# Kernel tuning notes

Measured on AMD Instinct MI355X. Metric: run time of the kernel, lower is better.

The kernel has to match this reference:

```python
import jax, jax.numpy as jnp
import numpy as np

L = 4        # routed layers
E = 12       # experts
NH = 4       # attention heads
C = 256      # hidden_dim
M = 128      # mlp_dim
TOPK = 1
LN_EPS = 1e-5


def setup_inputs() -> dict:
    key = jax.random.key(0)
    ks = jax.random.split(key, 16)
    B, H, W = 128, 14, 14

    def w(k, shape, s=0.02):
        return jax.random.normal(k, shape, dtype=jnp.float32) * s

    return {
        'stem_out': jax.random.normal(ks[0], (B, C, H, W), dtype=jnp.float32),
        'gate_w': w(ks[1], (L, C, E)), 'gate_b': jnp.zeros((L, E), jnp.float32),
        'ln1_g': jnp.ones((L, E, C), jnp.float32), 'ln1_b': jnp.zeros((L, E, C), jnp.float32),
        'wq': w(ks[2], (L, E, C, C)), 'bq': jnp.zeros((L, E, C), jnp.float32),
        'wk': w(ks[3], (L, E, C, C)), 'bk': jnp.zeros((L, E, C), jnp.float32),
        'wv': w(ks[4], (L, E, C, C)), 'bv': jnp.zeros((L, E, C), jnp.float32),
        'wo': w(ks[5], (L, E, C, C)), 'bo': jnp.zeros((L, E, C), jnp.float32),
        'ln2_g': jnp.ones((L, E, C), jnp.float32), 'ln2_b': jnp.zeros((L, E, C), jnp.float32),
        'w1': w(ks[6], (L, E, C, M)), 'b1': jnp.zeros((L, E, M), jnp.float32),
        'w2': w(ks[7], (L, E, M, C)), 'b2': jnp.zeros((L, E, C), jnp.float32),
    }


def _ln(x, g, b):
    mu = x.mean(axis=-1, keepdims=True)
    var = ((x - mu) ** 2).mean(axis=-1, keepdims=True)
    return (x - mu) * jax.lax.rsqrt(var + LN_EPS) * g + b


def _vit_block(x, p):
    # x: (B, H, W, C); p: per-expert params (no expert axis)
    B, H, W, Cc = x.shape
    d = Cc // NH
    h = _ln(x, p['g1'], p['bb1'])
    q = h @ p['wq'] + p['bq']
    k = h @ p['wk'] + p['bk']
    v = h @ p['wv'] + p['bv']

    def split(t):  # (B,H,W,C) -> (B, NH, H, W, d)
        return jnp.transpose(t.reshape(B, H, W, NH, d), (0, 3, 1, 2, 4))

    q, k, v = split(q), split(k), split(v)
    # attention is computed PER ROW h (over the W axis), matching the
    # original matmul(q, k.transpose(-2,-1)) on b n h w d tensors
    scale = jnp.asarray(d, x.dtype) ** 0.5
    scores = jnp.einsum('bnhqd,bnhkd->bnhqk', q, k) / scale
    attn = jax.nn.softmax(scores, axis=-1)
    o = jnp.einsum('bnhqk,bnhkd->bnhqd', attn, v)
    o = jnp.transpose(o, (0, 2, 3, 1, 4)).reshape(B, H, W, Cc)
    o = o @ p['wo'] + p['bo']
    x = x + o
    m = _ln(x, p['g2'], p['bb2'])
    m = jax.nn.gelu(m @ p['w1'] + p['b1'], approximate=False) @ p['w2'] + p['b2']
    return x + m


def reference(stem_out, gate_w, gate_b, ln1_g, ln1_b, wq, bq, wk, bk, wv, bv,
              wo, bo, ln2_g, ln2_b, w1, b1, w2, b2):
    x = jnp.transpose(stem_out, (0, 2, 3, 1))  # (B, H, W, C)
    B = x.shape[0]
    outputs_map, probs_list, idx_list = [], [], []
    for li in range(L):
        router_in = x.mean(axis=(1, 2))                 # (B, C)
        logits = router_in @ gate_w[li] + gate_b[li]    # (B, E)
        all_probs = jax.nn.softmax(logits, axis=-1)
        tk_p, tk_i = jax.lax.top_k(all_probs, TOPK)
        tk_p = tk_p / (tk_p.sum(axis=-1, keepdims=True) + 1e-8)
        # dense combine weights (B, E): scatter top-k weights per batch row
        w_be = jnp.zeros((B, E), x.dtype).at[jnp.arange(B)[:, None], tk_i].add(tk_p)
        p_li = {'g1': ln1_g[li], 'bb1': ln1_b[li],
                'wq': wq[li], 'bq': bq[li], 'wk': wk[li], 'bk': bk[li],
                'wv': wv[li], 'bv': bv[li], 'wo': wo[li], 'bo': bo[li],
                'g2': ln2_g[li], 'bb2': ln2_b[li],
                'w1': w1[li], 'b1': b1[li], 'w2': w2[li], 'b2': b2[li]}
        expert_outs = jax.vmap(lambda pp: _vit_block(x, pp))(p_li)  # (E,B,H,W,C)
        x = jnp.einsum('ebhwc,be->bhwc', expert_outs, w_be)
        outputs_map.append(jax.lax.stop_gradient(x))
        probs_list.append(all_probs)
        idx_list.append(tk_i)
    return (jnp.stack(outputs_map, axis=0),          # (4, B, H, W, C)
            jnp.concatenate(probs_list, axis=0),     # (4B, E)
            jnp.concatenate(idx_list, axis=0))       # (4B, top_k)
```

## Files before the change

kernel.cpp:

```cpp
#include <hip/hip_runtime.h>
#include <hip/hip_bf16.h>

#define LNUM 4
#define ENUM 12
#define CH 256
#define MLP 128
#define HW 196
#define BNUM 128
#define ROWLEN 14
#define MTOT (BNUM * HW)
#define TM 64
#define MAXTILE 416

#define PK_WQ 0
#define PK_WK 786432
#define PK_WV 1572864
#define PK_WO 2359296
#define PK_W1 3145728
#define PK_W2 3538944
#define PK_TOTAL 3932160

using bf16x8 = __attribute__((ext_vector_type(8))) short;
using f32x4 = __attribute__((ext_vector_type(4))) float;

__device__ inline unsigned short f2bf(float v) {
  __hip_bfloat16 b = __float2bfloat16(v);
  return *reinterpret_cast<unsigned short*>(&b);
}
__device__ inline float bf2f(unsigned short u) {
  union { unsigned int i; float f; } cv;
  cv.i = ((unsigned int)u) << 16;
  return cv.f;
}
__device__ inline void split_bf(float v, unsigned short& hi, unsigned short& lo) {
  hi = f2bf(v);
  lo = f2bf(v - bf2f(hi));
}
__device__ inline void gload16(const void* g, void* l) {
  __builtin_amdgcn_global_load_lds(
      (const __attribute__((address_space(1))) unsigned int*)g,
      (__attribute__((address_space(3))) unsigned int*)l, 16, 0, 0);
}

__global__ __launch_bounds__(256) void transpose_stem(const float* __restrict__ stem,
                                                      float* __restrict__ x) {
  __shared__ float tile[32][33];
  int b = blockIdx.z;
  int c0 = blockIdx.x * 32;
  int p0 = blockIdx.y * 32;
  int tx = threadIdx.x;
  int ty = threadIdx.y;
  for (int i = ty; i < 32; i += 8) {
    int c = c0 + i, p = p0 + tx;
    if (p < HW) tile[i][tx] = stem[(size_t)b * CH * HW + (size_t)c * HW + p];
  }
  __syncthreads();
  for (int i = ty; i < 32; i += 8) {
    int p = p0 + i, c = c0 + tx;
    if (p < HW) x[(size_t)b * HW * CH + (size_t)p * CH + c] = tile[tx][i];
  }
}

__global__ __launch_bounds__(256) void router_kernel(
    const float* __restrict__ x, const float* __restrict__ gate_w,
    const float* __restrict__ gate_b, float* __restrict__ probs_out,
    float* __restrict__ idx_out, float* __restrict__ weight,
    int* __restrict__ eidx, int li) {
  int b = blockIdx.x;
  int c = threadIdx.x;
  const float* xb = x + (size_t)b * HW * CH;
  float s = 0.f;
  for (int p = 0; p < HW; ++p) s += xb[(size_t)p * CH + c];
  __shared__ float r[CH];
  r[c] = s * (1.0f / (float)HW);
  __syncthreads();
  __shared__ float logits[ENUM];
  if (c < ENUM) {
    float acc = gate_b[li * ENUM + c];
    for (int k = 0; k < CH; ++k)
      acc += r[k] * gate_w[((size_t)li * CH + k) * ENUM + c];
    logits[c] = acc;
  }
  __syncthreads();
  if (c == 0) {
    float mx = logits[0]; int am = 0;
    for (int e = 1; e < ENUM; ++e) if (logits[e] > mx) { mx = logits[e]; am = e; }
    float pr[ENUM]; float den = 0.f;
    for (int e = 0; e < ENUM; ++e) { pr[e] = expf(logits[e] - mx); den += pr[e]; }
    float inv = 1.0f / den;
    for (int e = 0; e < ENUM; ++e) pr[e] *= inv;
    for (int e = 0; e < ENUM; ++e)
      probs_out[(size_t)(li * BNUM + b) * ENUM + e] = pr[e];
    idx_out[li * BNUM + b] = (float)am;
    float pmax = pr[am];
    weight[b] = pmax / (pmax + 1e-8f);
    eidx[b] = am;
  }
}

__global__ void route_plan(const int* __restrict__ eidx, int* __restrict__ perm,
                           int* __restrict__ tile_e, int* __restrict__ tile_row0,
                           int* __restrict__ tile_rows) {
  __shared__ int cnt[ENUM], start[ENUM];
  int t = threadIdx.x;
  if (t < ENUM) {
    int c = 0;
    for (int b = 0; b < BNUM; ++b) if (eidx[b] == t) ++c;
    cnt[t] = c;
  }
  __syncthreads();
  if (t == 0) {
    int s = 0;
    for (int e = 0; e < ENUM; ++e) { start[e] = s; s += cnt[e]; }
  }
  __syncthreads();
  if (t < ENUM) {
    int pos = start[t];
    for (int b = 0; b < BNUM; ++b) if (eidx[b] == t) perm[pos++] = b;
  }
  __syncthreads();
  if (t == 0) {
    int tile = 0;
    for (int e = 0; e < ENUM; ++e) {
      int rows = cnt[e] * HW;
      int row0 = start[e] * HW;
      int off = 0;
      while (off < rows) {
        tile_e[tile] = e;
        tile_row0[tile] = row0 + off;
        int rem = rows - off;
        tile_rows[tile] = rem < TM ? rem : TM;
        ++tile; off += TM;
      }
    }
    for (; tile < MAXTILE; ++tile) { tile_rows[tile] = 0; tile_e[tile] = 0; tile_row0[tile] = 0; }
  }
}

__global__ __launch_bounds__(256) void prepack(
    const float* __restrict__ wq, const float* __restrict__ wk,
    const float* __restrict__ wv, const float* __restrict__ wo,
    const float* __restrict__ w1, const float* __restrict__ w2,
    unsigned short* __restrict__ Phi, unsigned short* __restrict__ Plo) {
  int e = blockIdx.z;
  int ts = blockIdx.y;
  int K = (ts == 5) ? 128 : 256;
  int N = (ts == 4) ? 128 : 256;
  int total = (K / 8) * N;
  int id = blockIdx.x * 256 + threadIdx.x;
  if (id >= total) return;
  const float* src;
  size_t dst0;
  switch (ts) {
    case 0: src = wq; dst0 = PK_WQ; break;
    case 1: src = wk; dst0 = PK_WK; break;
    case 2: src = wv; dst0 = PK_WV; break;
    case 3: src = wo; dst0 = PK_WO; break;
    case 4: src = w1; dst0 = PK_W1; break;
    default: src = w2; dst0 = PK_W2; break;
  }
  src += (size_t)e * K * N;
  dst0 += (size_t)e * K * N;
  int n = id % N;
  int kg = id / N;
  const float* sp = src + (size_t)kg * 8 * N + n;
  unsigned short hs[8], ls[8];
#pragma unroll
  for (int j = 0; j < 8; ++j) split_bf(sp[(size_t)j * N], hs[j], ls[j]);
  uint4 ph, pl;
  ph.x = hs[0] | ((unsigned)hs[1] << 16); ph.y = hs[2] | ((unsigned)hs[3] << 16);
  ph.z = hs[4] | ((unsigned)hs[5] << 16); ph.w = hs[6] | ((unsigned)hs[7] << 16);
  pl.x = ls[0] | ((unsigned)ls[1] << 16); pl.y = ls[2] | ((unsigned)ls[3] << 16);
  pl.z = ls[4] | ((unsigned)ls[5] << 16); pl.w = ls[6] | ((unsigned)ls[7] << 16);
  size_t o = dst0 + (size_t)(kg * N + n) * 8;
  *reinterpret_cast<uint4*>(Phi + o) = ph;
  *reinterpret_cast<uint4*>(Plo + o) = pl;
}

__global__ __launch_bounds__(256) void ln_kernel(
    const float* __restrict__ xin, unsigned short* __restrict__ hhi,
    unsigned short* __restrict__ hlo,
    const float* __restrict__ g, const float* __restrict__ bta,
    const int* __restrict__ eidx, const int* __restrict__ perm, int li) {
  int t = blockIdx.x;
  int s = t / HW, p = t - s * HW;
  int b = perm[s];
  int e = eidx[b];
  int c = threadIdx.x;
  float vx = xin[((size_t)b * HW + p) * CH + c];
  float sm = vx;
  for (int off = 32; off > 0; off >>= 1) sm += __shfl_down(sm, off, 64);
  __shared__ float wsum[4];
  __shared__ float red[2];
  int wid = c >> 6, lane = c & 63;
  if (lane == 0) wsum[wid] = sm;
  __syncthreads();
  if (c == 0) red[0] = (wsum[0] + wsum[1] + wsum[2] + wsum[3]) * (1.0f / (float)CH);
  __syncthreads();
  float mu = red[0];
  float d = vx - mu;
  float s2 = d * d;
  for (int off = 32; off > 0; off >>= 1) s2 += __shfl_down(s2, off, 64);
  if (lane == 0) wsum[wid] = s2;
  __syncthreads();
  if (c == 0) red[1] = (wsum[0] + wsum[1] + wsum[2] + wsum[3]) * (1.0f / (float)CH);
  __syncthreads();
  float rs = rsqrtf(red[1] + 1e-5f);
  size_t gb = ((size_t)li * ENUM + e) * CH + c;
  float hv = d * rs * g[gb] + bta[gb];
  unsigned short hi, lo;
  split_bf(hv, hi, lo);
  hhi[(size_t)t * CH + c] = hi;
  hlo[(size_t)t * CH + c] = lo;
}

template <int EPI, int NT, int KDIM>
__global__ __launch_bounds__(256) void gemm_mfma(
    const unsigned short* __restrict__ Ahi, const unsigned short* __restrict__ Alo,
    const unsigned short* __restrict__ Whi, const unsigned short* __restrict__ Wlo,
    size_t wbase, size_t wstride,
    const float* __restrict__ B0, const float* __restrict__ B1p, const float* __restrict__ B2p,
    float* __restrict__ O0, float* __restrict__ O1p, float* __restrict__ O2p,
    unsigned short* __restrict__ Omhi, unsigned short* __restrict__ Omlo,
    float* __restrict__ X, const float* __restrict__ wgt,
    const int* __restrict__ tile_e, const int* __restrict__ tile_row0,
    const int* __restrict__ tile_rows, const int* __restrict__ perm, int li) {
  constexpr int NX = NT / 128;
  int rows = tile_rows[blockIdx.y];
  if (rows <= 0) return;
  int row0 = tile_row0[blockIdx.y];
  int e = tile_e[blockIdx.y];
  int cb = blockIdx.x / NX;
  int ncol0 = (blockIdx.x % NX) * 128;

  const float* Bt = (EPI == 0) ? (cb == 0 ? B0 : (cb == 1 ? B1p : B2p)) : B0;
  float* Oo = (EPI == 0) ? (cb == 0 ? O0 : (cb == 1 ? O1p : O2p)) : O0;
  size_t woff = wbase + (size_t)cb * wstride + (size_t)e * (KDIM * NT);
  const unsigned short* Wh = Whi + woff;
  const unsigned short* Wl = Wlo + woff;
  const float* bias = Bt + ((size_t)li * ENUM + e) * NT + ncol0;

  __shared__ unsigned short Ash[4][TM][8], Asl[4][TM][8];
  __shared__ unsigned short Bsh[4][128][8], Bsl[4][128][8];

  int tid = threadIdx.x;
  int lane = tid & 63, w = tid >> 6;
  int wr = w >> 1, wc = w & 1;
  int r0w = wr * 32, c0w = wc * 64;
  int lrow = lane & 15, lk = lane >> 4;

  int arow = row0 + (lane < rows ? lane : 0);
  const unsigned short* gAh = Ahi + (size_t)arow * KDIM + w * 8;
  const unsigned short* gAl = Alo + (size_t)arow * KDIM + w * 8;

  f32x4 acc[2][4];
#pragma unroll
  for (int i = 0; i < 2; ++i)
#pragma unroll
    for (int j = 0; j < 4; ++j) acc[i][j] = (f32x4){0.f, 0.f, 0.f, 0.f};

#pragma unroll
  for (int t = 0; t < KDIM / 32; ++t) {
    int k0 = t * 32;
    gload16(gAh + k0, &Ash[w][0][0]);
    gload16(gAl + k0, &Asl[w][0][0]);
    const unsigned short* gBh = Wh + ((size_t)(t * 4 + w) * NT + ncol0 + lane) * 8;
    const unsigned short* gBl = Wl + ((size_t)(t * 4 + w) * NT + ncol0 + lane) * 8;
    gload16(gBh, &Bsh[w][0][0]);
    gload16(gBh + 64 * 8, &Bsh[w][64][0]);
    gload16(gBl, &Bsl[w][0][0]);
    gload16(gBl + 64 * 8, &Bsl[w][64][0]);
    __syncthreads();
    bf16x8 ah[2], al[2], bh[4], bl[4];
#pragma unroll
    for (int fi = 0; fi < 2; ++fi) {
      ah[fi] = *reinterpret_cast<const bf16x8*>(&Ash[lk][r0w + fi * 16 + lrow][0]);
      al[fi] = *reinterpret_cast<const bf16x8*>(&Asl[lk][r0w + fi * 16 + lrow][0]);
    }
#pragma unroll
    for (int fj = 0; fj < 4; ++fj) {
      bh[fj] = *reinterpret_cast<const bf16x8*>(&Bsh[lk][c0w + fj * 16 + lrow][0]);
      bl[fj] = *reinterpret_cast<const bf16x8*>(&Bsl[lk][c0w + fj * 16 + lrow][0]);
    }
#pragma unroll
    for (int fi = 0; fi < 2; ++fi)
#pragma unroll
      for (int fj = 0; fj < 4; ++fj) {
        acc[fi][fj] = __builtin_amdgcn_mfma_f32_16x16x32_bf16(ah[fi], bh[fj], acc[fi][fj], 0, 0, 0);
        acc[fi][fj] = __builtin_amdgcn_mfma_f32_16x16x32_bf16(ah[fi], bl[fj], acc[fi][fj], 0, 0, 0);
        acc[fi][fj] = __builtin_amdgcn_mfma_f32_16x16x32_bf16(al[fi], bh[fj], acc[fi][fj], 0, 0, 0);
      }
    __syncthreads();
  }

#pragma unroll
  for (int fi = 0; fi < 2; ++fi) {
#pragma unroll
    for (int r = 0; r < 4; ++r) {
      int row_l = r0w + fi * 16 + lk * 4 + r;
      if (row_l >= rows) continue;
      int rg = row0 + row_l;
      int bsrt = 0; size_t gxb = 0; float wr_ = 1.f;
      if (EPI >= 2) {
        int s = rg / HW, p = rg - s * HW;
        bsrt = perm[s];
        gxb = ((size_t)bsrt * HW + p) * CH;
        if (EPI == 3) wr_ = wgt[bsrt];
      }
#pragma unroll
      for (int fj = 0; fj < 4; ++fj) {
        int col = c0w + fj * 16 + lrow;
        int ocol = ncol0 + col;
        float v = acc[fi][fj][r] + bias[col];
        if (EPI == 0) {
          Oo[(size_t)rg * NT + ocol] = v;
        } else if (EPI == 1) {
          float gl = 0.5f * v * (1.0f + erff(v * 0.70710678118654752f));
          unsigned short hi, lo;
          split_bf(gl, hi, lo);
          Omhi[(size_t)rg * MLP + ocol] = hi;
          Omlo[(size_t)rg * MLP + ocol] = lo;
        } else if (EPI == 2) {
          X[gxb + ocol] += v;
        } else {
          float vv = (v + X[gxb + ocol]) * wr_;
          X[gxb + ocol] = vv;
          O0[gxb + ocol] = vv;
        }
      }
    }
  }
}

__global__ __launch_bounds__(256) void attn_kernel(
    const float* __restrict__ q, const float* __restrict__ k,
    const float* __restrict__ v, unsigned short* __restrict__ ohi,
    unsigned short* __restrict__ olo) {
  int br = blockIdx.x;
  int b = br / ROWLEN, row = br % ROWLEN;
  size_t base = ((size_t)b * HW + (size_t)row * ROWLEN) * CH;
  __shared__ float qs[ROWLEN][CH + 1];
  __shared__ float ks[ROWLEN][CH + 1];
  __shared__ float vs[ROWLEN][CH + 1];
  __shared__ float sc[4][ROWLEN][ROWLEN];
  int tid = threadIdx.x;
  for (int w = 0; w < ROWLEN; ++w) {
    qs[w][tid] = q[base + (size_t)w * CH + tid];
    ks[w][tid] = k[base + (size_t)w * CH + tid];
    vs[w][tid] = v[base + (size_t)w * CH + tid];
  }
  __syncthreads();
  for (int sidx = tid; sidx < 4 * ROWLEN * ROWLEN; sidx += 256) {
    int n = sidx / (ROWLEN * ROWLEN);
    int rem = sidx % (ROWLEN * ROWLEN);
    int i = rem / ROWLEN, j = rem % ROWLEN;
    const float* qp = &qs[i][n * 64];
    const float* kp = &ks[j][n * 64];
    float s = 0.f;
#pragma unroll
    for (int d = 0; d < 64; ++d) s = fmaf(qp[d], kp[d], s);
    sc[n][i][j] = s * 0.125f;
  }
  __syncthreads();
  if (tid < 4 * ROWLEN) {
    int n = tid / ROWLEN, i = tid % ROWLEN;
    float mx = sc[n][i][0];
    for (int j = 1; j < ROWLEN; ++j) mx = fmaxf(mx, sc[n][i][j]);
    float ex[ROWLEN]; float den = 0.f;
    for (int j = 0; j < ROWLEN; ++j) { ex[j] = expf(sc[n][i][j] - mx); den += ex[j]; }
    float inv = 1.0f / den;
    for (int j = 0; j < ROWLEN; ++j) sc[n][i][j] = ex[j] * inv;
  }
  __syncthreads();
  int n = tid / 64;
  for (int i = 0; i < ROWLEN; ++i) {
    float s = 0.f;
#pragma unroll
    for (int j = 0; j < ROWLEN; ++j) s = fmaf(sc[n][i][j], vs[j][tid], s);
    unsigned short hi, lo;
    split_bf(s, hi, lo);
    ohi[base + (size_t)i * CH + tid] = hi;
    olo[base + (size_t)i * CH + tid] = lo;
  }
}

extern "C" void kernel_launch(void* const* d_in, const int* in_sizes, int n_in,
                              void* d_out, int out_size, void* d_ws, size_t ws_size,
                              hipStream_t stream) {
  const float* stem = (const float*)d_in[0];
  const float* gate_w = (const float*)d_in[1];
  const float* gate_b = (const float*)d_in[2];
  const float* ln1_g = (const float*)d_in[3];
  const float* ln1_b = (const float*)d_in[4];
  const float* wq = (const float*)d_in[5];
  const float* bq = (const float*)d_in[6];
  const float* wk = (const float*)d_in[7];
  const float* bk = (const float*)d_in[8];
  const float* wv = (const float*)d_in[9];
  const float* bv = (const float*)d_in[10];
  const float* wo = (const float*)d_in[11];
  const float* bo = (const float*)d_in[12];
  const float* ln2_g = (const float*)d_in[13];
  const float* ln2_b = (const float*)d_in[14];
  const float* w1 = (const float*)d_in[15];
  const float* b1 = (const float*)d_in[16];
  const float* w2 = (const float*)d_in[17];
  const float* b2 = (const float*)d_in[18];

  float* out = (float*)d_out;
  float* ws = (float*)d_ws;
  const size_t IMG = (size_t)BNUM * HW * CH;
  float* x = ws;
  unsigned short* h_hi = (unsigned short*)(ws + IMG);
  unsigned short* h_lo = h_hi + (size_t)MTOT * CH;
  float* q = ws + 2 * IMG;
  float* k = ws + 3 * IMG;
  float* v = ws + 4 * IMG;
  unsigned short* m_hi = (unsigned short*)q;
  unsigned short* m_lo = m_hi + (size_t)MTOT * MLP;
  unsigned short* Whi_p = (unsigned short*)(ws + 5 * IMG);
  unsigned short* Wlo_p = Whi_p + PK_TOTAL;
  float* weight = ws + 5 * IMG + PK_TOTAL;
  int* eidx = (int*)(weight + BNUM);
  int* perm = eidx + BNUM;
  int* tile_e = perm + BNUM;
  int* tile_row0 = tile_e + MAXTILE;
  int* tile_rows = tile_row0 + MAXTILE;

  float* probs_out = out + 4 * IMG;
  float* idx_out = probs_out + (size_t)LNUM * BNUM * ENUM;

  transpose_stem<<<dim3(8, 7, BNUM), dim3(32, 8), 0, stream>>>(stem, x);

  for (int li = 0; li < LNUM; ++li) {
    router_kernel<<<BNUM, 256, 0, stream>>>(x, gate_w, gate_b, probs_out, idx_out,
                                            weight, eidx, li);
    route_plan<<<1, 64, 0, stream>>>(eidx, perm, tile_e, tile_row0, tile_rows);
    prepack<<<dim3(32, 6, ENUM), 256, 0, stream>>>(
        wq + (size_t)li * ENUM * CH * CH, wk + (size_t)li * ENUM * CH * CH,
        wv + (size_t)li * ENUM * CH * CH, wo + (size_t)li * ENUM * CH * CH,
        w1 + (size_t)li * ENUM * CH * MLP, w2 + (size_t)li * ENUM * MLP * CH,
        Whi_p, Wlo_p);
    ln_kernel<<<MTOT, 256, 0, stream>>>(x, h_hi, h_lo, ln1_g, ln1_b, eidx, perm, li);
    gemm_mfma<0, 256, 256><<<dim3(6, MAXTILE), 256, 0, stream>>>(
        h_hi, h_lo, Whi_p, Wlo_p, PK_WQ, (size_t)(ENUM * CH * CH),
        bq, bk, bv, q, k, v, nullptr, nullptr, nullptr, nullptr,
        tile_e, tile_row0, tile_rows, perm, li);
    attn_kernel<<<BNUM * ROWLEN, 256, 0, stream>>>(q, k, v, h_hi, h_lo);
    gemm_mfma<2, 256, 256><<<dim3(2, MAXTILE), 256, 0, stream>>>(
        h_hi, h_lo, Whi_p, Wlo_p, PK_WO, 0,
        bo, nullptr, nullptr, nullptr, nullptr, nullptr, nullptr, nullptr,
        x, nullptr, tile_e, tile_row0, tile_rows, perm, li);
    ln_kernel<<<MTOT, 256, 0, stream>>>(x, h_hi, h_lo, ln2_g, ln2_b, eidx, perm, li);
    gemm_mfma<1, 128, 256><<<dim3(1, MAXTILE), 256, 0, stream>>>(
        h_hi, h_lo, Whi_p, Wlo_p, PK_W1, 0,
        b1, nullptr, nullptr, nullptr, nullptr, nullptr, m_hi, m_lo,
        nullptr, nullptr, tile_e, tile_row0, tile_rows, perm, li);
    gemm_mfma<3, 256, 128><<<dim3(2, MAXTILE), 256, 0, stream>>>(
        m_hi, m_lo, Whi_p, Wlo_p, PK_W2, 0,
        b2, nullptr, nullptr, out + (size_t)li * IMG, nullptr, nullptr,
        nullptr, nullptr, x, weight, tile_e, tile_row0, tile_rows, perm, li);
  }
}
```

Baseline: 1.039 ms.

## Double-buffer GEMM shared-memory tiles and use one wavefront per LayerNorm token

```diff
diff --git a/kernel.cpp b/kernel.cpp
--- a/kernel.cpp
+++ b/kernel.cpp
@@ -182,36 +182,37 @@
     unsigned short* __restrict__ hlo,
     const float* __restrict__ g, const float* __restrict__ bta,
     const int* __restrict__ eidx, const int* __restrict__ perm, int li) {
-  int t = blockIdx.x;
-  int s = t / HW, p = t - s * HW;
+  int tok = blockIdx.x * 4 + (threadIdx.x >> 6);
+  int lane = threadIdx.x & 63;
+  int s = tok / HW, p = tok - s * HW;
   int b = perm[s];
   int e = eidx[b];
-  int c = threadIdx.x;
-  float vx = xin[((size_t)b * HW + p) * CH + c];
-  float sm = vx;
-  for (int off = 32; off > 0; off >>= 1) sm += __shfl_down(sm, off, 64);
-  __shared__ float wsum[4];
-  __shared__ float red[2];
-  int wid = c >> 6, lane = c & 63;
-  if (lane == 0) wsum[wid] = sm;
-  __syncthreads();
-  if (c == 0) red[0] = (wsum[0] + wsum[1] + wsum[2] + wsum[3]) * (1.0f / (float)CH);
-  __syncthreads();
-  float mu = red[0];
-  float d = vx - mu;
-  float s2 = d * d;
-  for (int off = 32; off > 0; off >>= 1) s2 += __shfl_down(s2, off, 64);
-  if (lane == 0) wsum[wid] = s2;
-  __syncthreads();
-  if (c == 0) red[1] = (wsum[0] + wsum[1] + wsum[2] + wsum[3]) * (1.0f / (float)CH);
-  __syncthreads();
-  float rs = rsqrtf(red[1] + 1e-5f);
-  size_t gb = ((size_t)li * ENUM + e) * CH + c;
-  float hv = d * rs * g[gb] + bta[gb];
-  unsigned short hi, lo;
-  split_bf(hv, hi, lo);
-  hhi[(size_t)t * CH + c] = hi;
-  hlo[(size_t)t * CH + c] = lo;
+  float4 vx = *reinterpret_cast<const float4*>(
+      &xin[((size_t)b * HW + p) * CH + lane * 4]);
+  float sm = vx.x + vx.y + vx.z + vx.w;
+#pragma unroll
+  for (int off = 1; off < 64; off <<= 1) sm += __shfl_xor(sm, off, 64);
+  float mu = sm * (1.0f / (float)CH);
+  float d0 = vx.x - mu, d1 = vx.y - mu, d2 = vx.z - mu, d3 = vx.w - mu;
+  float s2 = d0 * d0 + d1 * d1 + d2 * d2 + d3 * d3;
+#pragma unroll
+  for (int off = 1; off < 64; off <<= 1) s2 += __shfl_xor(s2, off, 64);
+  float rs = rsqrtf(s2 * (1.0f / (float)CH) + 1e-5f);
+  size_t gb = ((size_t)li * ENUM + e) * CH + lane * 4;
+  float4 gg = *reinterpret_cast<const float4*>(&g[gb]);
+  float4 bb = *reinterpret_cast<const float4*>(&bta[gb]);
+  float h0 = d0 * rs * gg.x + bb.x;
+  float h1 = d1 * rs * gg.y + bb.y;
+  float h2 = d2 * rs * gg.z + bb.z;
+  float h3 = d3 * rs * gg.w + bb.w;
+  ushort4 vh, vl;
+  split_bf(h0, vh.x, vl.x);
+  split_bf(h1, vh.y, vl.y);
+  split_bf(h2, vh.z, vl.z);
+  split_bf(h3, vh.w, vl.w);
+  size_t ob = (size_t)tok * CH + lane * 4;
+  *reinterpret_cast<ushort4*>(&hhi[ob]) = vh;
+  *reinterpret_cast<ushort4*>(&hlo[ob]) = vl;
 }
 
 template <int EPI, int NT, int KDIM>
@@ -226,6 +227,7 @@
     const int* __restrict__ tile_e, const int* __restrict__ tile_row0,
     const int* __restrict__ tile_rows, const int* __restrict__ perm, int li) {
   constexpr int NX = NT / 128;
+  constexpr int NSTEP = KDIM / 32;
   int rows = tile_rows[blockIdx.y];
   if (rows <= 0) return;
   int row0 = tile_row0[blockIdx.y];
@@ -240,8 +242,8 @@
   const unsigned short* Wl = Wlo + woff;
   const float* bias = Bt + ((size_t)li * ENUM + e) * NT + ncol0;
 
-  __shared__ unsigned short Ash[4][TM][8], Asl[4][TM][8];
-  __shared__ unsigned short Bsh[4][128][8], Bsl[4][128][8];
+  __shared__ unsigned short Ash[2][4][TM][8], Asl[2][4][TM][8];
+  __shared__ unsigned short Bsh[2][4][128][8], Bsl[2][4][128][8];
 
   int tid = threadIdx.x;
   int lane = tid & 63, w = tid >> 6;
@@ -253,34 +255,44 @@
   const unsigned short* gAh = Ahi + (size_t)arow * KDIM + w * 8;
   const unsigned short* gAl = Alo + (size_t)arow * KDIM + w * 8;
 
+#define STAGE(T, BUF)                                                          \
+  {                                                                            \
+    int k0_ = (T) * 32;                                                        \
+    gload16(gAh + k0_, &Ash[BUF][w][0][0]);                                    \
+    gload16(gAl + k0_, &Asl[BUF][w][0][0]);                                    \
+    const unsigned short* gBh_ =                                               \
+        Wh + ((size_t)((T) * 4 + w) * NT + ncol0 + lane) * 8;                  \
+    const unsigned short* gBl_ =                                               \
+        Wl + ((size_t)((T) * 4 + w) * NT + ncol0 + lane) * 8;                  \
+    gload16(gBh_, &Bsh[BUF][w][0][0]);                                         \
+    gload16(gBh_ + 64 * 8, &Bsh[BUF][w][64][0]);                               \
+    gload16(gBl_, &Bsl[BUF][w][0][0]);                                         \
+    gload16(gBl_ + 64 * 8, &Bsl[BUF][w][64][0]);                               \
+  }
+
   f32x4 acc[2][4];
 #pragma unroll
   for (int i = 0; i < 2; ++i)
 #pragma unroll
     for (int j = 0; j < 4; ++j) acc[i][j] = (f32x4){0.f, 0.f, 0.f, 0.f};
 
-#pragma unroll
-  for (int t = 0; t < KDIM / 32; ++t) {
-    int k0 = t * 32;
-    gload16(gAh + k0, &Ash[w][0][0]);
-    gload16(gAl + k0, &Asl[w][0][0]);
-    const unsigned short* gBh = Wh + ((size_t)(t * 4 + w) * NT + ncol0 + lane) * 8;
-    const unsigned short* gBl = Wl + ((size_t)(t * 4 + w) * NT + ncol0 + lane) * 8;
-    gload16(gBh, &Bsh[w][0][0]);
-    gload16(gBh + 64 * 8, &Bsh[w][64][0]);
-    gload16(gBl, &Bsl[w][0][0]);
-    gload16(gBl + 64 * 8, &Bsl[w][64][0]);
-    __syncthreads();
+  STAGE(0, 0);
+  __syncthreads();
+
+#pragma unroll
+  for (int t = 0; t < NSTEP; ++t) {
+    const int buf = t & 1;
+    if (t + 1 < NSTEP) STAGE(t + 1, buf ^ 1);
     bf16x8 ah[2], al[2], bh[4], bl[4];
 #pragma unroll
     for (int fi = 0; fi < 2; ++fi) {
-      ah[fi] = *reinterpret_cast<const bf16x8*>(&Ash[lk][r0w + fi * 16 + lrow][0]);
-      al[fi] = *reinterpret_cast<const bf16x8*>(&Asl[lk][r0w + fi * 16 + lrow][0]);
+      ah[fi] = *reinterpret_cast<const bf16x8*>(&Ash[buf][lk][r0w + fi * 16 + lrow][0]);
+      al[fi] = *reinterpret_cast<const bf16x8*>(&Asl[buf][lk][r0w + fi * 16 + lrow][0]);
     }
 #pragma unroll
     for (int fj = 0; fj < 4; ++fj) {
-      bh[fj] = *reinterpret_cast<const bf16x8*>(&Bsh[lk][c0w + fj * 16 + lrow][0]);
-      bl[fj] = *reinterpret_cast<const bf16x8*>(&Bsl[lk][c0w + fj * 16 + lrow][0]);
+      bh[fj] = *reinterpret_cast<const bf16x8*>(&Bsh[buf][lk][c0w + fj * 16 + lrow][0]);
+      bl[fj] = *reinterpret_cast<const bf16x8*>(&Bsl[buf][lk][c0w + fj * 16 + lrow][0]);
     }
 #pragma unroll
     for (int fi = 0; fi < 2; ++fi)
@@ -292,6 +304,7 @@
       }
     __syncthreads();
   }
+#undef STAGE
 
 #pragma unroll
   for (int fi = 0; fi < 2; ++fi) {
@@ -441,7 +454,7 @@
         wv + (size_t)li * ENUM * CH * CH, wo + (size_t)li * ENUM * CH * CH,
         w1 + (size_t)li * ENUM * CH * MLP, w2 + (size_t)li * ENUM * MLP * CH,
         Whi_p, Wlo_p);
-    ln_kernel<<<MTOT, 256, 0, stream>>>(x, h_hi, h_lo, ln1_g, ln1_b, eidx, perm, li);
+    ln_kernel<<<MTOT / 4, 256, 0, stream>>>(x, h_hi, h_lo, ln1_g, ln1_b, eidx, perm, li);
     gemm_mfma<0, 256, 256><<<dim3(6, MAXTILE), 256, 0, stream>>>(
         h_hi, h_lo, Whi_p, Wlo_p, PK_WQ, (size_t)(ENUM * CH * CH),
         bq, bk, bv, q, k, v, nullptr, nullptr, nullptr, nullptr,
@@ -451,7 +464,7 @@
         h_hi, h_lo, Whi_p, Wlo_p, PK_WO, 0,
         bo, nullptr, nullptr, nullptr, nullptr, nullptr, nullptr, nullptr,
         x, nullptr, tile_e, tile_row0, tile_rows, perm, li);
-    ln_kernel<<<MTOT, 256, 0, stream>>>(x, h_hi, h_lo, ln2_g, ln2_b, eidx, perm, li);
+    ln_kernel<<<MTOT / 4, 256, 0, stream>>>(x, h_hi, h_lo, ln2_g, ln2_b, eidx, perm, li);
     gemm_mfma<1, 128, 256><<<dim3(1, MAXTILE), 256, 0, stream>>>(
         h_hi, h_lo, Whi_p, Wlo_p, PK_W1, 0,
         b1, nullptr, nullptr, nullptr, nullptr, nullptr, m_hi, m_lo,
```

Measured after the change: 1.046 ms. Within noise of the previous version (+0.7%).
